# Kernel tuning notes

Measured on AMD Instinct MI355X. Metric: run time of the kernel, lower is better.

## Reference

```python
import jax, jax.numpy as jnp
import numpy as np

D_MODEL = 1024
NUM_HEADS = 16
DK = D_MODEL // NUM_HEADS  # 64


def setup_inputs() -> dict:
    key = jax.random.key(0)
    kx, kq, kk, kv, ko = jax.random.split(key, 5)
    B, S = 4, 2048
    # xavier-uniform-ish scale for square [d_model, d_model] matrices
    bound = float(np.sqrt(6.0 / (D_MODEL + D_MODEL)))
    uni = lambda k: jax.random.uniform(k, (D_MODEL, D_MODEL), jnp.float32, -bound, bound)
    return {
        "x": jax.random.normal(kx, (B, S, D_MODEL), jnp.float32),
        "q_heads": uni(kq),
        "k_heads": uni(kk),
        "v_heads": uni(kv),
        "output_proj": uni(ko),
    }


def reference(x, q_heads, k_heads, v_heads, output_proj):
    B, S, _ = x.shape
    # projections: x @ W.T, split into heads -> [B, H, S, dk]
    def proj(W):
        return (x @ W.T).reshape(B, S, NUM_HEADS, DK).transpose(0, 2, 1, 3)
    q, k, v = proj(q_heads), proj(k_heads), proj(v_heads)
    scale = 1.0 / jnp.sqrt(jnp.asarray(DK, x.dtype))
    scores = jnp.einsum("bhqd,bhkd->bhqk", q, k) * scale  # [B,H,S,S]
    causal = jnp.triu(jnp.ones((S, S), bool), k=1)
    scores = jnp.where(causal, jnp.asarray(-jnp.inf, scores.dtype), scores)
    attn = jax.nn.softmax(scores, axis=-1)
    out = jnp.einsum("bhqk,bhkd->bhqd", attn, v)  # [B,H,S,dk]
    out = out.transpose(0, 2, 1, 3).reshape(B, S, D_MODEL)
    return out @ output_proj.T
```

## Files before the change

kernel.cpp:

```cpp
#include <hip/hip_runtime.h>
#include <hip/hip_bf16.h>

#define AS1 __attribute__((address_space(1)))
#define AS3 __attribute__((address_space(3)))

typedef __hip_bfloat16 bf16;
typedef short bf16x8 __attribute__((ext_vector_type(8)));
typedef float f32x4 __attribute__((ext_vector_type(4)));

static constexpr int D = 1024, S = 2048, NB = 4, NH = 16, DK = 64;
static constexpr int M = NB * S;

__device__ __forceinline__ void gload16(void* lds_dst, const void* gsrc) {
  __builtin_amdgcn_global_load_lds((const AS1 void*)gsrc, (AS3 void*)lds_dst, 16, 0, 0);
}

__global__ void cvt_bf16_kernel(const float* __restrict__ src, bf16* __restrict__ dst, int n) {
  int i = (blockIdx.x * blockDim.x + threadIdx.x) * 4;
  int stride = gridDim.x * blockDim.x * 4;
  for (; i < n; i += stride) {
    float4 v = *(const float4*)(src + i);
    union { bf16 h[4]; uint2 u; } t;
    t.h[0] = __float2bfloat16(v.x);
    t.h[1] = __float2bfloat16(v.y);
    t.h[2] = __float2bfloat16(v.z);
    t.h[3] = __float2bfloat16(v.w);
    *(uint2*)(dst + i) = t.u;
  }
}

template <int MODE>
__global__ __launch_bounds__(256)
void gemm_bt(const bf16* __restrict__ A, const bf16* __restrict__ Bw,
             void* __restrict__ out, int K, int ldc, float scale) {
  __shared__ __align__(16) char lds[32768];
  char* Asm = lds;
  char* Bsm = lds + 16384;
  const int tid = threadIdx.x;
  const int w = tid >> 6, l = tid & 63;
  const int ql = l & 15, g = l >> 4;
  const int rowA = blockIdx.x * 128;
  const int rowB = blockIdx.y * 128;
  const int wr = (w >> 1) * 64, wc = (w & 1) * 64;

  f32x4 acc[4][4] = {};

  for (int k0 = 0; k0 < K; k0 += 64) {
#pragma unroll
    for (int i = 0; i < 4; ++i) {
      int o = ((i * 4 + w) << 10) + (l << 4);
      int row = o >> 7;
      int u = ((o >> 4) & 7) ^ (row & 7);
      gload16(Asm + ((i * 4 + w) << 10), A + (size_t)(rowA + row) * K + k0 + (u << 3));
      gload16(Bsm + ((i * 4 + w) << 10), Bw + (size_t)(rowB + row) * K + k0 + (u << 3));
    }
    __syncthreads();
#pragma unroll
    for (int kk = 0; kk < 2; ++kk) {
      bf16x8 af[4], bfr[4];
#pragma unroll
      for (int m = 0; m < 4; ++m) {
        int row = wr + m * 16 + ql;
        int sub = ((kk << 2) + g) ^ (row & 7);
        af[m] = *(const bf16x8*)(Asm + row * 128 + sub * 16);
      }
#pragma unroll
      for (int n = 0; n < 4; ++n) {
        int row = wc + n * 16 + ql;
        int sub = ((kk << 2) + g) ^ (row & 7);
        bfr[n] = *(const bf16x8*)(Bsm + row * 128 + sub * 16);
      }
#pragma unroll
      for (int m = 0; m < 4; ++m)
#pragma unroll
        for (int n = 0; n < 4; ++n)
          acc[m][n] = __builtin_amdgcn_mfma_f32_16x16x32_bf16(af[m], bfr[n], acc[m][n], 0, 0, 0);
    }
    __syncthreads();
  }

#pragma unroll
  for (int m = 0; m < 4; ++m)
#pragma unroll
    for (int n = 0; n < 4; ++n)
#pragma unroll
      for (int r = 0; r < 4; ++r) {
        int gm = rowA + wr + m * 16 + g * 4 + r;
        int gn = rowB + wc + n * 16 + ql;
        float v = acc[m][n][r] * scale;
        if (MODE == 0) {
          int b = gm >> 11, s = gm & 2047, h = gn >> 6, d = gn & 63;
          ((bf16*)out)[(((size_t)(b * 16 + h) * S) + s) * DK + d] = __float2bfloat16(v);
        } else if (MODE == 1) {
          int b = gn >> 11, s = gn & 2047;
          ((bf16*)out)[((size_t)b * 1024 + gm) * S + s] = __float2bfloat16(v);
        } else {
          ((float*)out)[(size_t)gm * ldc + gn] = v;
        }
      }
}

__global__ __launch_bounds__(256)
void attn_kernel(const bf16* __restrict__ Q, const bf16* __restrict__ Km,
                 const bf16* __restrict__ Vt, bf16* __restrict__ O) {
  __shared__ __align__(16) char P[4][2][2048];
  const int tid = threadIdx.x;
  const int w = tid >> 6, l = tid & 63;
  const int ql = l & 15, g = l >> 4;
  const int id = blockIdx.x;
  const int bh = (id & 7) + 8 * (id >> 6);
  const int x = (id >> 3) & 7;
  const int p = x + 8 * w;
  const int swz = (ql & 7) << 4;
  const float L2E = 1.44269504f;
  const float THR = 8.0f;

  const bf16* Qb = Q + (size_t)bh * S * DK;
  const bf16* Kb = Km + (size_t)bh * S * DK;
  const bf16* Vb = Vt + (size_t)bh * DK * S;
  const int bo = bh >> 4, hh = bh & 15;
  bf16* Ob = O + (size_t)bo * S * D + hh * 64;

  for (int round = 0; round < 2; ++round) {
    const int j = round ? 63 - p : p;
    const int qbase = j << 5;
    const int kv_end = qbase + 32;

    bf16x8 qf[2][2];
#pragma unroll
    for (int sub = 0; sub < 2; ++sub)
#pragma unroll
      for (int kk = 0; kk < 2; ++kk)
        qf[sub][kk] = *(const bf16x8*)(Qb + (size_t)(qbase + sub * 16 + ql) * DK + kk * 32 + g * 8);

    f32x4 oacc[2][4] = {};
    float mrow[2] = {-3e38f, -3e38f};
    float lrow[2] = {0.f, 0.f};

    for (int kv0 = 0; kv0 < kv_end; kv0 += 64) {
      const bool last = (kv0 + 64 >= kv_end);

      f32x4 st[2][4];
#pragma unroll
      for (int sub = 0; sub < 2; ++sub)
#pragma unroll
        for (int mt = 0; mt < 4; ++mt) st[sub][mt] = f32x4{0.f, 0.f, 0.f, 0.f};
      __builtin_amdgcn_s_setprio(1);
#pragma unroll
      for (int kk = 0; kk < 2; ++kk) {
        bf16x8 kf[4];
#pragma unroll
        for (int mt = 0; mt < 4; ++mt)
          kf[mt] = *(const bf16x8*)(Kb + (size_t)(kv0 + mt * 16 + ql) * DK + kk * 32 + g * 8);
#pragma unroll
        for (int sub = 0; sub < 2; ++sub)
#pragma unroll
          for (int mt = 0; mt < 4; ++mt)
            st[sub][mt] = __builtin_amdgcn_mfma_f32_16x16x32_bf16(kf[mt], qf[sub][kk], st[sub][mt], 0, 0, 0);
      }
      __builtin_amdgcn_s_setprio(0);

      bf16x8 vf[2][4];
#pragma unroll
      for (int kk = 0; kk < 2; ++kk)
#pragma unroll
        for (int n = 0; n < 4; ++n)
          vf[kk][n] = *(const bf16x8*)(Vb + (size_t)(n * 16 + ql) * S + kv0 + kk * 32 + g * 8);

#pragma unroll
      for (int sub = 0; sub < 2; ++sub) {
        const int qpos = qbase + sub * 16 + ql;
        if (last) {
#pragma unroll
          for (int mt = 0; mt < 4; ++mt)
#pragma unroll
            for (int r = 0; r < 4; ++r) {
              int kvpos = kv0 + mt * 16 + g * 4 + r;
              if (kvpos > qpos) st[sub][mt][r] = -3e38f;
            }
        }
        float tmax = st[sub][0][0];
#pragma unroll
        for (int mt = 0; mt < 4; ++mt)
#pragma unroll
          for (int r = 0; r < 4; ++r) tmax = fmaxf(tmax, st[sub][mt][r]);
        if (__any(tmax > mrow[sub] + THR)) {
          float rm = tmax;
          rm = fmaxf(rm, __shfl_xor(rm, 16, 64));
          rm = fmaxf(rm, __shfl_xor(rm, 32, 64));
          float mnew = fmaxf(mrow[sub], rm);
          float sc = exp2f((mrow[sub] - mnew) * L2E);
          mrow[sub] = mnew;
          lrow[sub] *= sc;
#pragma unroll
          for (int r = 0; r < 4; ++r) {
            float scr = __shfl(sc, g * 4 + r, 16);
#pragma unroll
            for (int n = 0; n < 4; ++n) oacc[sub][n][r] *= scr;
          }
        }
        float psum = 0.f;
#pragma unroll
        for (int mt = 0; mt < 4; ++mt) {
          union { ushort us[4]; uint2 u; } pk;
#pragma unroll
          for (int r = 0; r < 4; ++r) {
            float pv = exp2f((st[sub][mt][r] - mrow[sub]) * L2E);
            psum += pv;
            union { bf16 b; ushort u; } cv;
            cv.b = __float2bfloat16(pv);
            pk.us[r] = cv.u;
          }
          *(uint2*)&P[w][sub][((ql << 7) + (mt << 5) + (g << 3)) ^ swz] = pk.u;
        }
        lrow[sub] += psum;
      }

      __builtin_amdgcn_s_setprio(1);
#pragma unroll
      for (int kk = 0; kk < 2; ++kk)
#pragma unroll
        for (int sub = 0; sub < 2; ++sub) {
          bf16x8 pa = *(const bf16x8*)&P[w][sub][((ql << 7) + (kk << 6) + (g << 4)) ^ swz];
#pragma unroll
          for (int n = 0; n < 4; ++n)
            oacc[sub][n] = __builtin_amdgcn_mfma_f32_16x16x32_bf16(pa, vf[kk][n], oacc[sub][n], 0, 0, 0);
        }
      __builtin_amdgcn_s_setprio(0);
    }

#pragma unroll
    for (int sub = 0; sub < 2; ++sub) {
      float lr = lrow[sub];
      lr += __shfl_xor(lr, 16, 64);
      lr += __shfl_xor(lr, 32, 64);
      float ldv[4];
#pragma unroll
      for (int r = 0; r < 4; ++r) ldv[r] = __shfl(lr, g * 4 + r, 16);
#pragma unroll
      for (int r = 0; r < 4; ++r) {
        int qrow = qbase + sub * 16 + g * 4 + r;
        float inv = 1.f / ldv[r];
#pragma unroll
        for (int n = 0; n < 4; ++n)
          Ob[(size_t)qrow * D + n * 16 + ql] = __float2bfloat16(oacc[sub][n][r] * inv);
      }
    }
  }
}

extern "C" void kernel_launch(void* const* d_in, const int* in_sizes, int n_in,
                              void* d_out, int out_size, void* d_ws, size_t ws_size,
                              hipStream_t stream) {
  const float* x  = (const float*)d_in[0];
  const float* wq = (const float*)d_in[1];
  const float* wk = (const float*)d_in[2];
  const float* wv = (const float*)d_in[3];
  const float* wo = (const float*)d_in[4];

  char* ws = (char*)d_ws;
  bf16* xb  = (bf16*)(ws);
  bf16* wqb = (bf16*)(ws + (16u << 20));
  bf16* wkb = (bf16*)(ws + (18u << 20));
  bf16* wvb = (bf16*)(ws + (20u << 20));
  bf16* wob = (bf16*)(ws + (22u << 20));
  bf16* Qb  = (bf16*)(ws + (24u << 20));
  bf16* Kb  = (bf16*)(ws + (40u << 20));
  bf16* Vtb = (bf16*)(ws + (56u << 20));
  bf16* Ob  = (bf16*)(ws + (72u << 20));

  cvt_bf16_kernel<<<2048, 256, 0, stream>>>(x, xb, M * D);
  cvt_bf16_kernel<<<1024, 256, 0, stream>>>(wq, wqb, D * D);
  cvt_bf16_kernel<<<1024, 256, 0, stream>>>(wk, wkb, D * D);
  cvt_bf16_kernel<<<1024, 256, 0, stream>>>(wv, wvb, D * D);
  cvt_bf16_kernel<<<1024, 256, 0, stream>>>(wo, wob, D * D);

  gemm_bt<0><<<dim3(M / 128, D / 128), 256, 0, stream>>>(xb, wqb, Qb, D, D, 0.125f);
  gemm_bt<0><<<dim3(M / 128, D / 128), 256, 0, stream>>>(xb, wkb, Kb, D, D, 1.0f);
  gemm_bt<1><<<dim3(D / 128, M / 128), 256, 0, stream>>>(wvb, xb, Vtb, D, D, 1.0f);

  attn_kernel<<<dim3(512), 256, 0, stream>>>(Qb, Kb, Vtb, Ob);

  gemm_bt<2><<<dim3(M / 128, D / 128), 256, 0, stream>>>(Ob, wob, d_out, D, D, 1.0f);
}
```

Baseline: 238.1 us.

## Prefetch next K tile, fold log2e into Q scale, tree-reduce softmax

The K fragments for the next KV tile are now loaded into registers during the current iteration, after the QK MFMAs, and the V loads are issued at the top of each iteration. The aim is to hide global-load latency behind the softmax and the PV MFMAs. The log2(e) factor is folded into the Q projection scale (0.125*1.4427), which removes a multiply per exponent. The max and sum reductions become pairwise trees to shorten dependency chains. The prefetch holds eight more bf16x8 vectors live, so register pressure and the risk of lower occupancy go up.

```diff
diff --git a/kernel.cpp b/kernel.cpp
--- a/kernel.cpp
+++ b/kernel.cpp
@@ -112,7 +112,6 @@
   const int x = (id >> 3) & 7;
   const int p = x + 8 * w;
   const int swz = (ql & 7) << 4;
-  const float L2E = 1.44269504f;
   const float THR = 8.0f;
 
   const bf16* Qb = Q + (size_t)bh * S * DK;
@@ -137,9 +136,23 @@
     float mrow[2] = {-3e38f, -3e38f};
     float lrow[2] = {0.f, 0.f};
 
+    bf16x8 kf[2][4];
+#pragma unroll
+    for (int kk = 0; kk < 2; ++kk)
+#pragma unroll
+      for (int mt = 0; mt < 4; ++mt)
+        kf[kk][mt] = *(const bf16x8*)(Kb + (size_t)(mt * 16 + ql) * DK + kk * 32 + g * 8);
+
     for (int kv0 = 0; kv0 < kv_end; kv0 += 64) {
       const bool last = (kv0 + 64 >= kv_end);
 
+      bf16x8 vf[2][4];
+#pragma unroll
+      for (int kk = 0; kk < 2; ++kk)
+#pragma unroll
+        for (int n = 0; n < 4; ++n)
+          vf[kk][n] = *(const bf16x8*)(Vb + (size_t)(n * 16 + ql) * S + kv0 + kk * 32 + g * 8);
+
       f32x4 st[2][4];
 #pragma unroll
       for (int sub = 0; sub < 2; ++sub)
@@ -147,25 +160,21 @@
         for (int mt = 0; mt < 4; ++mt) st[sub][mt] = f32x4{0.f, 0.f, 0.f, 0.f};
       __builtin_amdgcn_s_setprio(1);
 #pragma unroll
-      for (int kk = 0; kk < 2; ++kk) {
-        bf16x8 kf[4];
-#pragma unroll
-        for (int mt = 0; mt < 4; ++mt)
-          kf[mt] = *(const bf16x8*)(Kb + (size_t)(kv0 + mt * 16 + ql) * DK + kk * 32 + g * 8);
+      for (int kk = 0; kk < 2; ++kk)
 #pragma unroll
         for (int sub = 0; sub < 2; ++sub)
 #pragma unroll
           for (int mt = 0; mt < 4; ++mt)
-            st[sub][mt] = __builtin_amdgcn_mfma_f32_16x16x32_bf16(kf[mt], qf[sub][kk], st[sub][mt], 0, 0, 0);
-      }
+            st[sub][mt] = __builtin_amdgcn_mfma_f32_16x16x32_bf16(kf[kk][mt], qf[sub][kk], st[sub][mt], 0, 0, 0);
       __builtin_amdgcn_s_setprio(0);
 
-      bf16x8 vf[2][4];
-#pragma unroll
-      for (int kk = 0; kk < 2; ++kk)
-#pragma unroll
-        for (int n = 0; n < 4; ++n)
-          vf[kk][n] = *(const bf16x8*)(Vb + (size_t)(n * 16 + ql) * S + kv0 + kk * 32 + g * 8);
+      if (!last) {
+#pragma unroll
+        for (int kk = 0; kk < 2; ++kk)
+#pragma unroll
+          for (int mt = 0; mt < 4; ++mt)
+            kf[kk][mt] = *(const bf16x8*)(Kb + (size_t)(kv0 + 64 + mt * 16 + ql) * DK + kk * 32 + g * 8);
+      }
 
 #pragma unroll
       for (int sub = 0; sub < 2; ++sub) {
@@ -179,17 +188,18 @@
               if (kvpos > qpos) st[sub][mt][r] = -3e38f;
             }
         }
-        float tmax = st[sub][0][0];
+        float tm[4];
 #pragma unroll
         for (int mt = 0; mt < 4; ++mt)
-#pragma unroll
-          for (int r = 0; r < 4; ++r) tmax = fmaxf(tmax, st[sub][mt][r]);
+          tm[mt] = fmaxf(fmaxf(st[sub][mt][0], st[sub][mt][1]),
+                         fmaxf(st[sub][mt][2], st[sub][mt][3]));
+        float tmax = fmaxf(fmaxf(tm[0], tm[1]), fmaxf(tm[2], tm[3]));
         if (__any(tmax > mrow[sub] + THR)) {
           float rm = tmax;
           rm = fmaxf(rm, __shfl_xor(rm, 16, 64));
           rm = fmaxf(rm, __shfl_xor(rm, 32, 64));
           float mnew = fmaxf(mrow[sub], rm);
-          float sc = exp2f((mrow[sub] - mnew) * L2E);
+          float sc = exp2f(mrow[sub] - mnew);
           mrow[sub] = mnew;
           lrow[sub] *= sc;
 #pragma unroll
@@ -199,21 +209,23 @@
             for (int n = 0; n < 4; ++n) oacc[sub][n][r] *= scr;
           }
         }
-        float psum = 0.f;
+        float ps[4];
 #pragma unroll
         for (int mt = 0; mt < 4; ++mt) {
+          float e0 = exp2f(st[sub][mt][0] - mrow[sub]);
+          float e1 = exp2f(st[sub][mt][1] - mrow[sub]);
+          float e2 = exp2f(st[sub][mt][2] - mrow[sub]);
+          float e3 = exp2f(st[sub][mt][3] - mrow[sub]);
+          ps[mt] = (e0 + e1) + (e2 + e3);
           union { ushort us[4]; uint2 u; } pk;
-#pragma unroll
-          for (int r = 0; r < 4; ++r) {
-            float pv = exp2f((st[sub][mt][r] - mrow[sub]) * L2E);
-            psum += pv;
-            union { bf16 b; ushort u; } cv;
-            cv.b = __float2bfloat16(pv);
-            pk.us[r] = cv.u;
-          }
+          union { bf16 b; ushort u; } cv;
+          cv.b = __float2bfloat16(e0); pk.us[0] = cv.u;
+          cv.b = __float2bfloat16(e1); pk.us[1] = cv.u;
+          cv.b = __float2bfloat16(e2); pk.us[2] = cv.u;
+          cv.b = __float2bfloat16(e3); pk.us[3] = cv.u;
           *(uint2*)&P[w][sub][((ql << 7) + (mt << 5) + (g << 3)) ^ swz] = pk.u;
         }
-        lrow[sub] += psum;
+        lrow[sub] += (ps[0] + ps[1]) + (ps[2] + ps[3]);
       }
 
       __builtin_amdgcn_s_setprio(1);
@@ -275,7 +287,7 @@
   cvt_bf16_kernel<<<1024, 256, 0, stream>>>(wv, wvb, D * D);
   cvt_bf16_kernel<<<1024, 256, 0, stream>>>(wo, wob, D * D);
 
-  gemm_bt<0><<<dim3(M / 128, D / 128), 256, 0, stream>>>(xb, wqb, Qb, D, D, 0.125f);
+  gemm_bt<0><<<dim3(M / 128, D / 128), 256, 0, stream>>>(xb, wqb, Qb, D, D, 0.18033688f);
   gemm_bt<0><<<dim3(M / 128, D / 128), 256, 0, stream>>>(xb, wkb, Kb, D, D, 1.0f);
   gemm_bt<1><<<dim3(D / 128, M / 128), 256, 0, stream>>>(wvb, xb, Vtb, D, D, 1.0f);
 
```

After: 239.4 us. No clear change (+0.5%).
